# Kernel optimization log

Measured on AMD Instinct MI355X. Metric: run time of the kernel, lower is better.

## Reference

```python
import jax, jax.numpy as jnp
import numpy as np
import itertools

B = 2          # batches
NB = 65536     # points per batch
G = 100        # voxel grid extent per axis
CIN = 32
COUT = 32
K3 = 27        # 3x3x3 kernel offsets
CENTER = 13    # (0,0,0) offset index


def setup_inputs() -> dict:
    rng = np.random.default_rng(0)
    grid = -np.ones((B, G, G, G), dtype=np.int64)
    coords = []
    for b in range(B):
        flat = np.sort(rng.choice(G ** 3, size=NB, replace=False))
        x = flat // (G * G)
        y = (flat // G) % G
        z = flat % G
        grid[b, x, y, z] = np.arange(NB) + b * NB
        coords.append(np.stack([np.full(NB, b), x, y, z], axis=1))
    C = np.concatenate(coords, axis=0)  # [N,4] batch,x,y,z (batch-contiguous)
    offs = np.array(list(itertools.product([-1, 0, 1], repeat=3)))  # [27,3], idx 13 == (0,0,0)
    nx = C[:, 1][:, None] + offs[:, 0][None]
    ny = C[:, 2][:, None] + offs[:, 1][None]
    nz = C[:, 3][:, None] + offs[:, 2][None]
    inb = (nx >= 0) & (nx < G) & (ny >= 0) & (ny < G) & (nz >= 0) & (nz < G)
    nb = grid[C[:, 0][:, None], np.clip(nx, 0, G - 1), np.clip(ny, 0, G - 1), np.clip(nz, 0, G - 1)]
    nbr = np.where(inb, nb, -1).astype(np.int32)  # [N,27], -1 = no neighbor voxel

    key = jax.random.key(0)
    k1, k2, k3, k4, k5 = jax.random.split(key, 5)
    scale = 1.0 / np.sqrt(K3 * CIN)
    return {
        "x_F": jax.random.normal(k1, (B * NB, CIN), dtype=jnp.float32),
        "W_ch": jax.random.normal(k2, (K3, CIN, COUT), dtype=jnp.float32) * scale,
        "b_ch": jax.random.normal(k3, (COUT,), dtype=jnp.float32) * 0.01,
        "W_dw": jax.random.normal(k4, (K3, COUT, COUT), dtype=jnp.float32) * scale,
        "b_dw": jax.random.normal(k5, (COUT,), dtype=jnp.float32) * 0.01,
        "nbr": jnp.asarray(nbr),
        "th": 1,
        "num_batches": B,
    }


def _sparse_conv(F, W, b, nbr, valid):
    # F:[N,Cin], W:[27,Cin,Cout], nbr:[N,27] (clamped gather + mask)
    idx = jnp.maximum(nbr, 0)
    g = jnp.where(valid[:, :, None], F[idx], 0.0)  # [N,27,Cin]
    out = jnp.einsum('nkc,kcd->nd', g, W)
    return out if b is None else out + b


def reference(x_F, W_ch, b_ch, W_dw, b_dw, nbr, th, num_batches):
    valid = nbr >= 0
    idx = jnp.maximum(nbr, 0)

    # Channel_code: 3x3x3 sparse conv with bias
    x = _sparse_conv(x_F, W_ch, b_ch, nbr, valid)  # [N,COUT]

    # correlation score: ones-kernel conv with center tap zeroed, over all channels
    s = x.sum(-1)  # [N]
    valid_nc = valid.at[:, CENTER].set(False)
    corr = jnp.where(valid_nc, s[idx], 0.0).sum(-1)
    corr_norm = (x * x).sum(-1)  # 1x1 ones-kernel conv on x*x
    corr = corr / corr_norm

    # per-batch topk -> strong/weak split (batch-contiguous equal-sized batches)
    N = x.shape[0]
    nb_pts = N // num_batches
    k = int(nb_pts * th / 3.21)
    corr_b = corr.reshape(num_batches, nb_pts)
    _, top_idx = jax.lax.top_k(corr_b, k)
    mask = jnp.zeros((num_batches, nb_pts), dtype=bool)
    mask = mask.at[jnp.arange(num_batches)[:, None], top_idx].set(True).reshape(-1)

    # dw conv restricted to the strong subset (neighbors must also be strong)
    valid_s = valid & mask[idx] & mask[:, None]
    strong = _sparse_conv(x, W_dw, b_dw, nbr, valid_s)

    # union: strong points take conv output, weak points keep x features
    union_F = jnp.where(mask[:, None], strong, x)
    return union_F + x  # out = out + x
```

## Files before the change

kernel.cpp:

```cpp
#include <hip/hip_runtime.h>

#define K3 27
#define CENTER 13
#define NC 32
#define NREP 32

__global__ __launch_bounds__(256) void conv1_kernel(
    const float* __restrict__ xF,
    const float* __restrict__ Wch,
    const float* __restrict__ bch,
    const int*   __restrict__ nbr,
    float*  __restrict__ xo,
    double* __restrict__ so,
    double* __restrict__ cno)
{
    __shared__ float Gs[2][128 * 32];
    const int t     = threadIdx.x;
    const int pbase = blockIdx.x << 7;
    const int dgu   = __builtin_amdgcn_readfirstlane(t >> 6);
    const int pp    = t & 63;
    const int sw    = pp & 7;
    const int srow  = t >> 1;
    const int sh    = t & 1;
    const int stsw  = srow & 7;

    float acc[2][8];
#pragma unroll
    for (int i = 0; i < 2; i++)
#pragma unroll
        for (int d = 0; d < 8; d++) acc[i][d] = 0.f;

    float4 stg[4];
    {
        const int j = nbr[(size_t)(pbase + srow) * K3];
        if (j >= 0) {
            const float4* src = (const float4*)(xF + (size_t)j * NC) + sh * 4;
#pragma unroll
            for (int m = 0; m < 4; m++) stg[m] = src[m];
        } else {
            const float4 z = make_float4(0.f, 0.f, 0.f, 0.f);
#pragma unroll
            for (int m = 0; m < 4; m++) stg[m] = z;
        }
    }

    for (int k = 0; k < K3; k++) {
        const int cur = k & 1;
        {
            float4* dst = (float4*)(Gs[cur] + srow * 32);
#pragma unroll
            for (int m = 0; m < 4; m++) dst[(4 * sh + m) ^ stsw] = stg[m];
        }
        __syncthreads();
        if (k + 1 < K3) {
            const int j = nbr[(size_t)(pbase + srow) * K3 + k + 1];
            if (j >= 0) {
                const float4* src = (const float4*)(xF + (size_t)j * NC) + sh * 4;
#pragma unroll
                for (int m = 0; m < 4; m++) stg[m] = src[m];
            } else {
                const float4 z = make_float4(0.f, 0.f, 0.f, 0.f);
#pragma unroll
                for (int m = 0; m < 4; m++) stg[m] = z;
            }
        }
        const float* __restrict__ Wk = Wch + k * (NC * NC) + dgu * 8;
#pragma unroll
        for (int cc = 0; cc < 8; ++cc) {
            const float4 g0 = ((const float4*)(Gs[cur] + (pp     ) * 32))[cc ^ sw];
            const float4 g1 = ((const float4*)(Gs[cur] + (pp + 64) * 32))[cc ^ sw];
#pragma unroll
            for (int c4 = 0; c4 < 4; c4++) {
                const float* wr = Wk + (cc * 4 + c4) * NC;
                const float4 wa = ((const float4*)wr)[0];
                const float4 wb = ((const float4*)wr)[1];
                const float wv[8] = {wa.x, wa.y, wa.z, wa.w, wb.x, wb.y, wb.z, wb.w};
                const float gv[2] = {(&g0.x)[c4], (&g1.x)[c4]};
#pragma unroll
                for (int i = 0; i < 2; i++)
#pragma unroll
                    for (int d = 0; d < 8; d++)
                        acc[i][d] = fmaf(gv[i], wv[d], acc[i][d]);
            }
        }
        __syncthreads();
    }

#pragma unroll
    for (int d = 0; d < 8; d++) {
        const float bv = bch[dgu * 8 + d];
#pragma unroll
        for (int i = 0; i < 2; i++) acc[i][d] += bv;
    }
#pragma unroll
    for (int i = 0; i < 2; i++) {
        const int p = pp + 64 * i;
        float4* dst = (float4*)(Gs[0] + p * 32);
        dst[(dgu * 2    ) ^ sw] = make_float4(acc[i][0], acc[i][1], acc[i][2], acc[i][3]);
        dst[(dgu * 2 + 1) ^ sw] = make_float4(acc[i][4], acc[i][5], acc[i][6], acc[i][7]);
    }
    __syncthreads();
    if (t < 128) {
        double sum = 0.0, sq = 0.0;
        const float4* row = (const float4*)(Gs[0] + t * 32);
        const int tsw = t & 7;
#pragma unroll
        for (int m = 0; m < 8; m++) {
            const float4 v = row[m ^ tsw];
            sum += (double)v.x + (double)v.y + (double)v.z + (double)v.w;
            sq  += (double)v.x * v.x + (double)v.y * v.y + (double)v.z * v.z + (double)v.w * v.w;
        }
        so[pbase + t]  = sum;
        cno[pbase + t] = sq;
    }
    {
        float4* xout = (float4*)(xo + (size_t)pbase * NC);
#pragma unroll
        for (int f = 0; f < 4; f++) {
            const int idx = f * 256 + t;
            const int row = idx >> 3;
            const int m   = idx & 7;
            xout[idx] = ((const float4*)(Gs[0] + row * 32))[m ^ (row & 7)];
        }
    }
}

__global__ __launch_bounds__(256) void corr_hist_kernel(
    const double* __restrict__ s,
    const double* __restrict__ cn,
    const int*    __restrict__ nbr,
    unsigned*     __restrict__ key,
    unsigned*     __restrict__ rep,
    int NBpts, int N)
{
    __shared__ int nlds[256 * K3];
    const int t     = threadIdx.x;
    const int pbase = blockIdx.x * 256;
    {
        const int* g = nbr + (size_t)pbase * K3;
#pragma unroll
        for (int i = 0; i < K3; i++) nlds[i * 256 + t] = g[i * 256 + t];
    }
    __syncthreads();
    const int n = pbase + t;

    int jj[K3];
#pragma unroll
    for (int k = 0; k < K3; k++) jj[k] = nlds[t * K3 + k];

    double v[K3];
#pragma unroll
    for (int k = 0; k < K3; k++) {
        if (k == CENTER) continue;
        const int j  = jj[k];
        const int ja = (j < 0) ? 0 : j;
        const double val = s[ja];
        v[k] = (j < 0) ? 0.0 : val;
    }
    double a0 = 0.0, a1 = 0.0, a2 = 0.0, a3 = 0.0;
#pragma unroll
    for (int k = 0; k < K3; k++) {
        if (k == CENTER) continue;
        const int c = k & 3;
        if (c == 0) a0 += v[k];
        else if (c == 1) a1 += v[k];
        else if (c == 2) a2 += v[k];
        else a3 += v[k];
    }
    const double sum = (a0 + a1) + (a2 + a3);

    const float corr = (float)(sum / cn[n]);
    const unsigned uu = __float_as_uint(corr);
    const unsigned u  = (uu & 0x80000000u) ? ~uu : (uu | 0x80000000u);
    key[n] = u;
    const int b = n / NBpts;
    const unsigned r = (unsigned)blockIdx.x & (NREP - 1);
    atomicAdd(&rep[(size_t)r * (2u * 65536u) + (size_t)b * 65536u + (u >> 16)], 1u);
}

__global__ __launch_bounds__(256) void reduce_rep_kernel(
    const unsigned* __restrict__ rep,
    unsigned*       __restrict__ hist_sum)
{
    const int g = blockIdx.x * 256 + threadIdx.x;
    unsigned sum = 0;
#pragma unroll
    for (int r = 0; r < NREP; r++)
        sum += rep[(size_t)r * (2u * 65536u) + g];
    hist_sum[g] = sum;
}

__global__ __launch_bounds__(1024) void scan_hi_kernel(
    const unsigned* __restrict__ hist,
    const int*      __restrict__ thp,
    unsigned*       __restrict__ selhi,
    int*            __restrict__ selrk,
    int NBpts)
{
    __shared__ unsigned ss[1024];
    const int b = blockIdx.x;
    const int t = threadIdx.x;
    const unsigned* h = hist + (size_t)b * 65536u + t * 64;
    unsigned sum = 0;
#pragma unroll 8
    for (int i = 0; i < 64; i++) sum += h[i];
    ss[t] = sum;
    __syncthreads();
    for (int off = 1; off < 1024; off <<= 1) {
        unsigned v = (t + off < 1024) ? ss[t + off] : 0u;
        __syncthreads();
        ss[t] += v;
        __syncthreads();
    }
    int k = (int)((double)NBpts * (double)thp[0] / 3.21);
    if (k < 1) k = 1;
    if (k > NBpts) k = NBpts;
    unsigned run = ss[t] - sum;
    for (int i = 63; i >= 0; --i) {
        const unsigned c = h[i];
        if ((int)run < k && k <= (int)(run + c)) {
            selhi[b] = (unsigned)(t * 64 + i);
            selrk[b] = k - (int)run;
        }
        run += c;
    }
}

__global__ __launch_bounds__(256) void hist_lo_kernel(
    const unsigned* __restrict__ key,
    const unsigned* __restrict__ selhi,
    unsigned*       __restrict__ hist2,
    int NBpts, int N)
{
    const int n = blockIdx.x * 256 + threadIdx.x;
    if (n >= N) return;
    const int b = n / NBpts;
    const unsigned u = key[n];
    if ((u >> 16) == selhi[b])
        atomicAdd(&hist2[(size_t)b * 65536u + (u & 0xFFFFu)], 1u);
}

__global__ __launch_bounds__(1024) void scan_lo_kernel(
    const unsigned* __restrict__ hist2,
    const unsigned* __restrict__ selhi,
    const int*      __restrict__ selrk,
    unsigned*       __restrict__ selT,
    int*            __restrict__ selr)
{
    __shared__ unsigned ss[1024];
    const int b = blockIdx.x;
    const int t = threadIdx.x;
    const unsigned* h = hist2 + (size_t)b * 65536u + t * 64;
    unsigned sum = 0;
#pragma unroll 8
    for (int i = 0; i < 64; i++) sum += h[i];
    ss[t] = sum;
    __syncthreads();
    for (int off = 1; off < 1024; off <<= 1) {
        unsigned v = (t + off < 1024) ? ss[t + off] : 0u;
        __syncthreads();
        ss[t] += v;
        __syncthreads();
    }
    const int k = selrk[b];
    unsigned run = ss[t] - sum;
    for (int i = 63; i >= 0; --i) {
        const unsigned c = h[i];
        if ((int)run < k && k <= (int)(run + c)) {
            selT[b] = (selhi[b] << 16) | (unsigned)(t * 64 + i);
            selr[b] = k - (int)run;
        }
        run += c;
    }
}

__global__ __launch_bounds__(256) void mask_kernel(
    const unsigned* __restrict__ key,
    const unsigned* __restrict__ selT,
    int* __restrict__ mask,
    int* __restrict__ eqcnt,
    int NBpts)
{
    __shared__ int wc[4];
    const int n = blockIdx.x * 256 + threadIdx.x;
    const int b = n / NBpts;
    const unsigned u = key[n];
    const unsigned T = selT[b];
    mask[n] = (u > T) ? 1 : 0;
    const unsigned long long bal = __ballot(u == T);
    const int lane = threadIdx.x & 63;
    const int wid  = threadIdx.x >> 6;
    if (lane == 0) wc[wid] = __popcll(bal);
    __syncthreads();
    if (threadIdx.x == 0) eqcnt[blockIdx.x] = wc[0] + wc[1] + wc[2] + wc[3];
}

__global__ __launch_bounds__(512) void scan_kernel(
    const int* __restrict__ in, int* __restrict__ out,
    int n, int seg, int* __restrict__ total)
{
    __shared__ int ss[512];
    const int t = threadIdx.x;
    const int v = (t < n) ? in[t] : 0;
    ss[t] = v;
    __syncthreads();
    for (int off = 1; off < seg; off <<= 1) {
        int a = ((t & (seg - 1)) >= off) ? ss[t - off] : 0;
        __syncthreads();
        ss[t] += a;
        __syncthreads();
    }
    if (t < n) out[t] = ss[t] - v;
    if (total != nullptr && t == n - 1) total[0] = ss[t];
}

__global__ __launch_bounds__(256) void eqfinal_kernel(
    const unsigned* __restrict__ key,
    const unsigned* __restrict__ selT,
    const int*      __restrict__ selr,
    const int*      __restrict__ eqoff,
    int* __restrict__ mask,
    int* __restrict__ mcnt,
    int NBpts)
{
    __shared__ int wc[4], wm[4];
    const int n = blockIdx.x * 256 + threadIdx.x;
    const int b = n / NBpts;
    const unsigned u = key[n];
    const unsigned T = selT[b];
    const bool gt = (u > T);
    const bool eq = (u == T);
    const unsigned long long bal = __ballot(eq);
    const int lane = threadIdx.x & 63;
    const int wid  = threadIdx.x >> 6;
    if (lane == 0) wc[wid] = __popcll(bal);
    __syncthreads();
    int base = eqoff[blockIdx.x];
    for (int w = 0; w < wid; w++) base += wc[w];
    bool keep = false;
    if (eq) {
        const int g = base + __popcll(bal & ((1ull << lane) - 1ull));
        keep = (g < selr[b]);
        if (keep) mask[n] = 1;
    }
    const unsigned long long balm = __ballot(gt || keep);
    if (lane == 0) wm[wid] = __popcll(balm);
    __syncthreads();
    if (threadIdx.x == 0) mcnt[blockIdx.x] = wm[0] + wm[1] + wm[2] + wm[3];
}

__global__ __launch_bounds__(256) void emit_kernel(
    const int* __restrict__ mask,
    const int* __restrict__ moff,
    int* __restrict__ list)
{
    __shared__ int wc[4];
    const int n = blockIdx.x * 256 + threadIdx.x;
    const bool m = mask[n] != 0;
    const unsigned long long bal = __ballot(m);
    const int lane = threadIdx.x & 63;
    const int wid  = threadIdx.x >> 6;
    if (lane == 0) wc[wid] = __popcll(bal);
    __syncthreads();
    int base = moff[blockIdx.x];
    for (int w = 0; w < wid; w++) base += wc[w];
    if (m) list[base + __popcll(bal & ((1ull << lane) - 1ull))] = n;
}

__global__ __launch_bounds__(256) void scale2_kernel(
    const float4* __restrict__ x, float4* __restrict__ out, int n4)
{
    const int i = blockIdx.x * 256 + threadIdx.x;
    if (i < n4) {
        const float4 v = x[i];
        out[i] = make_float4(v.x + v.x, v.y + v.y, v.z + v.z, v.w + v.w);
    }
}

__global__ __launch_bounds__(256) void conv2_kernel(
    const float* __restrict__ x,
    const float* __restrict__ Wdw,
    const float* __restrict__ bdw,
    const int*   __restrict__ nbr,
    const int*   __restrict__ mask,
    const int*   __restrict__ list,
    const int*   __restrict__ cnt,
    float* __restrict__ out)
{
    __shared__ float Gs[2][128 * 32];
    const int t     = threadIdx.x;
    const int base  = blockIdx.x << 7;
    const int count = *cnt;
    if (base >= count) return;
    const int dgu   = __builtin_amdgcn_readfirstlane(t >> 6);
    const int pp    = t & 63;
    const int sw    = pp & 7;
    const int srow  = t >> 1;
    const int sh    = t & 1;
    const int stsw  = srow & 7;
    const int sp    = (base + srow < count) ? list[base + srow] : -1;

    float acc[2][8];
#pragma unroll
    for (int i = 0; i < 2; i++)
#pragma unroll
        for (int d = 0; d < 8; d++) acc[i][d] = 0.f;

    float4 stg[4];
    {
        const int j = (sp >= 0) ? nbr[(size_t)sp * K3] : -1;
        const bool v = (j >= 0) && (mask[j] != 0);
        if (v) {
            const float4* src = (const float4*)(x + (size_t)j * NC) + sh * 4;
#pragma unroll
            for (int m = 0; m < 4; m++) stg[m] = src[m];
        } else {
            const float4 z = make_float4(0.f, 0.f, 0.f, 0.f);
#pragma unroll
            for (int m = 0; m < 4; m++) stg[m] = z;
        }
    }

    for (int k = 0; k < K3; k++) {
        const int cur = k & 1;
        {
            float4* dst = (float4*)(Gs[cur] + srow * 32);
#pragma unroll
            for (int m = 0; m < 4; m++) dst[(4 * sh + m) ^ stsw] = stg[m];
        }
        __syncthreads();
        if (k + 1 < K3) {
            const int j = (sp >= 0) ? nbr[(size_t)sp * K3 + k + 1] : -1;
            const bool v = (j >= 0) && (mask[j] != 0);
            if (v) {
                const float4* src = (const float4*)(x + (size_t)j * NC) + sh * 4;
#pragma unroll
                for (int m = 0; m < 4; m++) stg[m] = src[m];
            } else {
                const float4 z = make_float4(0.f, 0.f, 0.f, 0.f);
#pragma unroll
                for (int m = 0; m < 4; m++) stg[m] = z;
            }
        }
        const float* __restrict__ Wk = Wdw + k * (NC * NC) + dgu * 8;
#pragma unroll
        for (int cc = 0; cc < 8; ++cc) {
            const float4 g0 = ((const float4*)(Gs[cur] + (pp     ) * 32))[cc ^ sw];
            const float4 g1 = ((const float4*)(Gs[cur] + (pp + 64) * 32))[cc ^ sw];
#pragma unroll
            for (int c4 = 0; c4 < 4; c4++) {
                const float* wr = Wk + (cc * 4 + c4) * NC;
                const float4 wa = ((const float4*)wr)[0];
                const float4 wb = ((const float4*)wr)[1];
                const float wv[8] = {wa.x, wa.y, wa.z, wa.w, wb.x, wb.y, wb.z, wb.w};
                const float gv[2] = {(&g0.x)[c4], (&g1.x)[c4]};
#pragma unroll
                for (int i = 0; i < 2; i++)
#pragma unroll
                    for (int d = 0; d < 8; d++)
                        acc[i][d] = fmaf(gv[i], wv[d], acc[i][d]);
            }
        }
        __syncthreads();
    }

#pragma unroll
    for (int i = 0; i < 2; i++) {
        const int p = pp + 64 * i;
        float4* dst = (float4*)(Gs[0] + p * 32);
        dst[(dgu * 2    ) ^ sw] = make_float4(acc[i][0], acc[i][1], acc[i][2], acc[i][3]);
        dst[(dgu * 2 + 1) ^ sw] = make_float4(acc[i][4], acc[i][5], acc[i][6], acc[i][7]);
    }
    __syncthreads();
    if (t < 128) {
        const int p = (base + t < count) ? list[base + t] : -1;
        if (p >= 0) {
            const float4* row = (const float4*)(Gs[0] + t * 32);
            const float4* xr  = (const float4*)(x + (size_t)p * NC);
            const float4* bb  = (const float4*)bdw;
            float4* orow = (float4*)(out + (size_t)p * NC);
            const int tsw = t & 7;
#pragma unroll
            for (int m = 0; m < 8; m++) {
                const float4 a  = row[m ^ tsw];
                const float4 bv = bb[m];
                const float4 xv = xr[m];
                orow[m] = make_float4((a.x + bv.x) + xv.x, (a.y + bv.y) + xv.y,
                                      (a.z + bv.z) + xv.z, (a.w + bv.w) + xv.w);
            }
        }
    }
}

extern "C" void kernel_launch(void* const* d_in, const int* in_sizes, int n_in,
                              void* d_out, int out_size, void* d_ws, size_t ws_size,
                              hipStream_t stream)
{
    const float* xF  = (const float*)d_in[0];
    const float* Wch = (const float*)d_in[1];
    const float* bch = (const float*)d_in[2];
    const float* Wdw = (const float*)d_in[3];
    const float* bdw = (const float*)d_in[4];
    const int*   nbr = (const int*)d_in[5];
    const int*   thp = (const int*)d_in[6];

    const int N = in_sizes[0] / NC;
    const int NBpts = N / 2;
    float* out = (float*)d_out;

    char* ws = (char*)d_ws;
    size_t off = 0;
    float*    x     = (float*)(ws + off);    off += (size_t)N * NC * sizeof(float);
    double*   s     = (double*)(ws + off);   off += (size_t)N * sizeof(double);
    double*   cn    = (double*)(ws + off);   off += (size_t)N * sizeof(double);
    unsigned* key   = (unsigned*)(ws + off); off += (size_t)N * sizeof(unsigned);
    int*      mask  = (int*)(ws + off);      off += (size_t)N * sizeof(int);
    int*      list  = (int*)(ws + off);      off += (size_t)N * sizeof(int);
    unsigned* hsum  = (unsigned*)(ws + off); off += 2u * 65536u * sizeof(unsigned);
    unsigned* hist2 = (unsigned*)(ws + off); off += 2u * 65536u * sizeof(unsigned);
    const size_t zero_bytes = 2u * 65536u * sizeof(unsigned);
    int*      cnt   = (int*)(ws + off);      off += 256;
    unsigned* selhi = (unsigned*)(ws + off); off += 256;
    int*      selrk = (int*)(ws + off);      off += 256;
    unsigned* selT  = (unsigned*)(ws + off); off += 256;
    int*      selr  = (int*)(ws + off);      off += 256;
    int*      eqcnt = (int*)(ws + off);      off += 512 * sizeof(int);
    int*      eqoff = (int*)(ws + off);      off += 512 * sizeof(int);
    int*      mcnt  = (int*)(ws + off);      off += 512 * sizeof(int);
    int*      moff  = (int*)(ws + off);      off += 512 * sizeof(int);

    const int nblk  = N / 256;
    const int cblk  = N / 128;

    unsigned* rep = (unsigned*)d_out;

    hipMemsetAsync(rep, 0, (size_t)out_size * sizeof(float), stream);
    hipMemsetAsync(hist2, 0, zero_bytes, stream);
    conv1_kernel<<<cblk, 256, 0, stream>>>(xF, Wch, bch, nbr, x, s, cn);
    corr_hist_kernel<<<nblk, 256, 0, stream>>>(s, cn, nbr, key, rep, NBpts, N);
    reduce_rep_kernel<<<nblk, 256, 0, stream>>>(rep, hsum);
    scan_hi_kernel<<<2, 1024, 0, stream>>>(hsum, thp, selhi, selrk, NBpts);
    hist_lo_kernel<<<nblk, 256, 0, stream>>>(key, selhi, hist2, NBpts, N);
    scan_lo_kernel<<<2, 1024, 0, stream>>>(hist2, selhi, selrk, selT, selr);
    mask_kernel<<<nblk, 256, 0, stream>>>(key, selT, mask, eqcnt, NBpts);
    scan_kernel<<<1, 512, 0, stream>>>(eqcnt, eqoff, nblk, 256, nullptr);
    eqfinal_kernel<<<nblk, 256, 0, stream>>>(key, selT, selr, eqoff, mask, mcnt, NBpts);
    scan_kernel<<<1, 512, 0, stream>>>(mcnt, moff, nblk, 512, cnt);
    emit_kernel<<<nblk, 256, 0, stream>>>(mask, moff, list);
    scale2_kernel<<<(N * NC / 4) / 256, 256, 0, stream>>>((const float4*)x, (float4*)out, N * NC / 4);
    conv2_kernel<<<cblk, 256, 0, stream>>>(x, Wdw, bdw, nbr, mask, list, cnt, out);
}
```

Measured before the change: 360.9 us.

## Re-tile conv thread mapping to one point x 16 channels and split corr gather

Both sparse-conv kernels now map each thread to one point and 16 output channels instead of two points and 8 channels. This halves the LDS gather reads per FMA and moves weight loads toward wider, wave-uniform float4 reads. The correlation/histogram kernel no longer stages the neighbour table in LDS. Instead four lanes per point each gather about 7 neighbour scores and combine them with shuffles, which spreads the gathers over four times as many threads. The atomics are now issued by only one lane in four, which may leave lanes idle.

Result: slower. 368.9 us (+2.2%).

```diff
diff --git a/kernel.cpp b/kernel.cpp
--- a/kernel.cpp
+++ b/kernel.cpp
@@ -17,18 +17,16 @@
     __shared__ float Gs[2][128 * 32];
     const int t     = threadIdx.x;
     const int pbase = blockIdx.x << 7;
-    const int dgu   = __builtin_amdgcn_readfirstlane(t >> 6);
-    const int pp    = t & 63;
-    const int sw    = pp & 7;
+    const int g16   = __builtin_amdgcn_readfirstlane(t >> 7);
+    const int p     = t & 127;
+    const int sw    = p & 7;
     const int srow  = t >> 1;
     const int sh    = t & 1;
     const int stsw  = srow & 7;
 
-    float acc[2][8];
-#pragma unroll
-    for (int i = 0; i < 2; i++)
-#pragma unroll
-        for (int d = 0; d < 8; d++) acc[i][d] = 0.f;
+    float acc[16];
+#pragma unroll
+    for (int d = 0; d < 16; d++) acc[d] = 0.f;
 
     float4 stg[4];
     {
@@ -64,40 +62,35 @@
                 for (int m = 0; m < 4; m++) stg[m] = z;
             }
         }
-        const float* __restrict__ Wk = Wch + k * (NC * NC) + dgu * 8;
+        const float* __restrict__ Wk = Wch + k * (NC * NC) + g16 * 16;
 #pragma unroll
         for (int cc = 0; cc < 8; ++cc) {
-            const float4 g0 = ((const float4*)(Gs[cur] + (pp     ) * 32))[cc ^ sw];
-            const float4 g1 = ((const float4*)(Gs[cur] + (pp + 64) * 32))[cc ^ sw];
+            const float4 g0 = ((const float4*)(Gs[cur] + p * 32))[cc ^ sw];
 #pragma unroll
             for (int c4 = 0; c4 < 4; c4++) {
-                const float* wr = Wk + (cc * 4 + c4) * NC;
-                const float4 wa = ((const float4*)wr)[0];
-                const float4 wb = ((const float4*)wr)[1];
-                const float wv[8] = {wa.x, wa.y, wa.z, wa.w, wb.x, wb.y, wb.z, wb.w};
-                const float gv[2] = {(&g0.x)[c4], (&g1.x)[c4]};
-#pragma unroll
-                for (int i = 0; i < 2; i++)
-#pragma unroll
-                    for (int d = 0; d < 8; d++)
-                        acc[i][d] = fmaf(gv[i], wv[d], acc[i][d]);
+                const float gc = (c4 == 0) ? g0.x : (c4 == 1) ? g0.y : (c4 == 2) ? g0.z : g0.w;
+                const float4* wr = (const float4*)(Wk + (cc * 4 + c4) * NC);
+#pragma unroll
+                for (int d4 = 0; d4 < 4; d4++) {
+                    const float4 w = wr[d4];
+                    acc[d4 * 4 + 0] = fmaf(gc, w.x, acc[d4 * 4 + 0]);
+                    acc[d4 * 4 + 1] = fmaf(gc, w.y, acc[d4 * 4 + 1]);
+                    acc[d4 * 4 + 2] = fmaf(gc, w.z, acc[d4 * 4 + 2]);
+                    acc[d4 * 4 + 3] = fmaf(gc, w.w, acc[d4 * 4 + 3]);
+                }
             }
         }
         __syncthreads();
     }
 
 #pragma unroll
-    for (int d = 0; d < 8; d++) {
-        const float bv = bch[dgu * 8 + d];
-#pragma unroll
-        for (int i = 0; i < 2; i++) acc[i][d] += bv;
-    }
-#pragma unroll
-    for (int i = 0; i < 2; i++) {
-        const int p = pp + 64 * i;
+    for (int d = 0; d < 16; d++) acc[d] += bch[g16 * 16 + d];
+    {
         float4* dst = (float4*)(Gs[0] + p * 32);
-        dst[(dgu * 2    ) ^ sw] = make_float4(acc[i][0], acc[i][1], acc[i][2], acc[i][3]);
-        dst[(dgu * 2 + 1) ^ sw] = make_float4(acc[i][4], acc[i][5], acc[i][6], acc[i][7]);
+#pragma unroll
+        for (int j = 0; j < 4; j++)
+            dst[(g16 * 4 + j) ^ sw] =
+                make_float4(acc[4 * j], acc[4 * j + 1], acc[4 * j + 2], acc[4 * j + 3]);
     }
     __syncthreads();
     if (t < 128) {
@@ -133,49 +126,38 @@
     unsigned*     __restrict__ rep,
     int NBpts, int N)
 {
-    __shared__ int nlds[256 * K3];
-    const int t     = threadIdx.x;
-    const int pbase = blockIdx.x * 256;
-    {
-        const int* g = nbr + (size_t)pbase * K3;
-#pragma unroll
-        for (int i = 0; i < K3; i++) nlds[i * 256 + t] = g[i * 256 + t];
-    }
-    __syncthreads();
-    const int n = pbase + t;
-
-    int jj[K3];
-#pragma unroll
-    for (int k = 0; k < K3; k++) jj[k] = nlds[t * K3 + k];
-
-    double v[K3];
-#pragma unroll
-    for (int k = 0; k < K3; k++) {
-        if (k == CENTER) continue;
-        const int j  = jj[k];
-        const int ja = (j < 0) ? 0 : j;
-        const double val = s[ja];
-        v[k] = (j < 0) ? 0.0 : val;
-    }
-    double a0 = 0.0, a1 = 0.0, a2 = 0.0, a3 = 0.0;
-#pragma unroll
-    for (int k = 0; k < K3; k++) {
-        if (k == CENTER) continue;
-        const int c = k & 3;
-        if (c == 0) a0 += v[k];
-        else if (c == 1) a1 += v[k];
-        else if (c == 2) a2 += v[k];
-        else a3 += v[k];
-    }
-    const double sum = (a0 + a1) + (a2 + a3);
-
-    const float corr = (float)(sum / cn[n]);
-    const unsigned uu = __float_as_uint(corr);
-    const unsigned u  = (uu & 0x80000000u) ? ~uu : (uu | 0x80000000u);
-    key[n] = u;
-    const int b = n / NBpts;
-    const unsigned r = (unsigned)blockIdx.x & (NREP - 1);
-    atomicAdd(&rep[(size_t)r * (2u * 65536u) + (size_t)b * 65536u + (u >> 16)], 1u);
+    const int t   = threadIdx.x;
+    const int sub = t & 3;
+    const int n   = blockIdx.x * 64 + (t >> 2);
+    const int k0  = sub * 7;
+    const int k1  = (k0 + 7 < K3) ? (k0 + 7) : K3;
+    const int* __restrict__ nrow = nbr + (size_t)n * K3;
+
+    int jj[7];
+#pragma unroll
+    for (int i = 0; i < 7; i++) {
+        const int k = k0 + i;
+        jj[i] = (k < k1 && k != CENTER) ? nrow[k] : -1;
+    }
+    double v[7];
+#pragma unroll
+    for (int i = 0; i < 7; i++) {
+        const int j = jj[i];
+        const double val = s[(j < 0) ? 0 : j];
+        v[i] = (j < 0) ? 0.0 : val;
+    }
+    double part = ((v[0] + v[1]) + (v[2] + v[3])) + ((v[4] + v[5]) + v[6]);
+    part += __shfl_xor(part, 1);
+    part += __shfl_xor(part, 2);
+    if (sub == 0) {
+        const float corr = (float)(part / cn[n]);
+        const unsigned uu = __float_as_uint(corr);
+        const unsigned u  = (uu & 0x80000000u) ? ~uu : (uu | 0x80000000u);
+        key[n] = u;
+        const int b = n / NBpts;
+        const unsigned r = (unsigned)blockIdx.x & (NREP - 1);
+        atomicAdd(&rep[(size_t)r * (2u * 65536u) + (size_t)b * 65536u + (u >> 16)], 1u);
+    }
 }
 
 __global__ __launch_bounds__(256) void reduce_rep_kernel(
@@ -392,19 +374,17 @@
     const int base  = blockIdx.x << 7;
     const int count = *cnt;
     if (base >= count) return;
-    const int dgu   = __builtin_amdgcn_readfirstlane(t >> 6);
-    const int pp    = t & 63;
-    const int sw    = pp & 7;
+    const int g16   = __builtin_amdgcn_readfirstlane(t >> 7);
+    const int p     = t & 127;
+    const int sw    = p & 7;
     const int srow  = t >> 1;
     const int sh    = t & 1;
     const int stsw  = srow & 7;
     const int sp    = (base + srow < count) ? list[base + srow] : -1;
 
-    float acc[2][8];
-#pragma unroll
-    for (int i = 0; i < 2; i++)
-#pragma unroll
-        for (int d = 0; d < 8; d++) acc[i][d] = 0.f;
+    float acc[16];
+#pragma unroll
+    for (int d = 0; d < 16; d++) acc[d] = 0.f;
 
     float4 stg[4];
     {
@@ -442,43 +422,42 @@
                 for (int m = 0; m < 4; m++) stg[m] = z;
             }
         }
-        const float* __restrict__ Wk = Wdw + k * (NC * NC) + dgu * 8;
+        const float* __restrict__ Wk = Wdw + k * (NC * NC) + g16 * 16;
 #pragma unroll
         for (int cc = 0; cc < 8; ++cc) {
-            const float4 g0 = ((const float4*)(Gs[cur] + (pp     ) * 32))[cc ^ sw];
-            const float4 g1 = ((const float4*)(Gs[cur] + (pp + 64) * 32))[cc ^ sw];
+            const float4 g0 = ((const float4*)(Gs[cur] + p * 32))[cc ^ sw];
 #pragma unroll
             for (int c4 = 0; c4 < 4; c4++) {
-                const float* wr = Wk + (cc * 4 + c4) * NC;
-                const float4 wa = ((const float4*)wr)[0];
-                const float4 wb = ((const float4*)wr)[1];
-                const float wv[8] = {wa.x, wa.y, wa.z, wa.w, wb.x, wb.y, wb.z, wb.w};
-                const float gv[2] = {(&g0.x)[c4], (&g1.x)[c4]};
-#pragma unroll
-                for (int i = 0; i < 2; i++)
-#pragma unroll
-                    for (int d = 0; d < 8; d++)
-                        acc[i][d] = fmaf(gv[i], wv[d], acc[i][d]);
+                const float gc = (c4 == 0) ? g0.x : (c4 == 1) ? g0.y : (c4 == 2) ? g0.z : g0.w;
+                const float4* wr = (const float4*)(Wk + (cc * 4 + c4) * NC);
+#pragma unroll
+                for (int d4 = 0; d4 < 4; d4++) {
+                    const float4 w = wr[d4];
+                    acc[d4 * 4 + 0] = fmaf(gc, w.x, acc[d4 * 4 + 0]);
+                    acc[d4 * 4 + 1] = fmaf(gc, w.y, acc[d4 * 4 + 1]);
+                    acc[d4 * 4 + 2] = fmaf(gc, w.z, acc[d4 * 4 + 2]);
+                    acc[d4 * 4 + 3] = fmaf(gc, w.w, acc[d4 * 4 + 3]);
+                }
             }
         }
         __syncthreads();
     }
 
-#pragma unroll
-    for (int i = 0; i < 2; i++) {
-        const int p = pp + 64 * i;
+    {
         float4* dst = (float4*)(Gs[0] + p * 32);
-        dst[(dgu * 2    ) ^ sw] = make_float4(acc[i][0], acc[i][1], acc[i][2], acc[i][3]);
-        dst[(dgu * 2 + 1) ^ sw] = make_float4(acc[i][4], acc[i][5], acc[i][6], acc[i][7]);
+#pragma unroll
+        for (int j = 0; j < 4; j++)
+            dst[(g16 * 4 + j) ^ sw] =
+                make_float4(acc[4 * j], acc[4 * j + 1], acc[4 * j + 2], acc[4 * j + 3]);
     }
     __syncthreads();
     if (t < 128) {
-        const int p = (base + t < count) ? list[base + t] : -1;
-        if (p >= 0) {
+        const int pt = (base + t < count) ? list[base + t] : -1;
+        if (pt >= 0) {
             const float4* row = (const float4*)(Gs[0] + t * 32);
-            const float4* xr  = (const float4*)(x + (size_t)p * NC);
+            const float4* xr  = (const float4*)(x + (size_t)pt * NC);
             const float4* bb  = (const float4*)bdw;
-            float4* orow = (float4*)(out + (size_t)p * NC);
+            float4* orow = (float4*)(out + (size_t)pt * NC);
             const int tsw = t & 7;
 #pragma unroll
             for (int m = 0; m < 8; m++) {
@@ -531,13 +510,14 @@
 
     const int nblk  = N / 256;
     const int cblk  = N / 128;
+    const int hblk  = N / 64;
 
     unsigned* rep = (unsigned*)d_out;
 
     hipMemsetAsync(rep, 0, (size_t)out_size * sizeof(float), stream);
     hipMemsetAsync(hist2, 0, zero_bytes, stream);
     conv1_kernel<<<cblk, 256, 0, stream>>>(xF, Wch, bch, nbr, x, s, cn);
-    corr_hist_kernel<<<nblk, 256, 0, stream>>>(s, cn, nbr, key, rep, NBpts, N);
+    corr_hist_kernel<<<hblk, 256, 0, stream>>>(s, cn, nbr, key, rep, NBpts, N);
     reduce_rep_kernel<<<nblk, 256, 0, stream>>>(rep, hsum);
     scan_hi_kernel<<<2, 1024, 0, stream>>>(hsum, thp, selhi, selrk, NBpts);
     hist_lo_kernel<<<nblk, 256, 0, stream>>>(key, selhi, hist2, NBpts, N);
```
